# Kernel optimization log

Hardware: AMD Instinct MI355X
Metric: run time of the kernel (lower is better)

## Reference

```python
import jax, jax.numpy as jnp
import numpy as np

B, N, E = 128, 196, 2048   # batch, num_features (14x14), encoder_dim
D, A = 512, 512            # decoder_dim, attention_dim


def setup_inputs() -> dict:
    key = jax.random.key(0)
    ks = jax.random.split(key, 8)
    s_e = 1.0 / np.sqrt(E)
    s_d = 1.0 / np.sqrt(D)
    s_a = 1.0 / np.sqrt(A)
    return {
        "encoder_out": jax.random.normal(ks[0], (B, N, E), dtype=jnp.float32),
        "decoder_hidden": jax.random.normal(ks[1], (B, D), dtype=jnp.float32),
        "We": jax.random.uniform(ks[2], (E, A), jnp.float32, -s_e, s_e),
        "be": jax.random.uniform(ks[3], (A,), jnp.float32, -s_e, s_e),
        "Wd": jax.random.uniform(ks[4], (D, A), jnp.float32, -s_d, s_d),
        "bd": jax.random.uniform(ks[5], (A,), jnp.float32, -s_d, s_d),
        "Wf": jax.random.uniform(ks[6], (A, 1), jnp.float32, -s_a, s_a),
        "bf": jax.random.uniform(ks[7], (1,), jnp.float32, -s_a, s_a),
    }


def reference(encoder_out, decoder_hidden, We, be, Wd, bd, Wf, bf):
    # att1: [B,N,A] projection of encoder features
    att1 = jnp.einsum('bne,ea->bna', encoder_out, We) + be
    # att2: [B,A] projection of decoder state, broadcast over N
    att2 = decoder_hidden @ Wd + bd
    att = jnp.tanh(att1 + att2[:, None, :])          # [B,N,A]
    scores = jnp.einsum('bna,ao->bno', att, Wf) + bf  # [B,N,1]
    alpha = jax.nn.softmax(scores, axis=1)            # softmax over num_features
    context = jnp.sum(encoder_out * alpha, axis=1)    # [B,E]
    return (context, alpha)
```

## Files before the change

### kernel.cpp

```cpp
#include <hip/hip_runtime.h>
#include <hip/hip_bf16.h>
#include <stdint.h>

#define B_   128
#define N_   196
#define E_   2048
#define D_   512
#define A_   512
#define MTOT (B_ * N_)

typedef short  short8  __attribute__((ext_vector_type(8)));
typedef float  floatx4 __attribute__((ext_vector_type(4)));

__device__ __forceinline__ unsigned short f2bf(float f) {
    union { float f; uint32_t u; } v; v.f = f;
    uint32_t r = v.u + 0x7FFFu + ((v.u >> 16) & 1u);
    return (unsigned short)(r >> 16);
}

__device__ __forceinline__ uint32_t pkbf(float a, float b) {
    uint32_t ua = __float_as_uint(a) + 0x8000u;
    uint32_t ub = __float_as_uint(b) + 0x8000u;
    return __builtin_amdgcn_perm(ub, ua, 0x07060302u);
}

__global__ void transcvt_k(const float* __restrict__ We, unsigned short* __restrict__ WeT) {
    __shared__ float tile[32][33];
    const int e0 = blockIdx.x * 32, a0 = blockIdx.y * 32;
    const int t = threadIdx.x, tc = t & 31, tr = t >> 5;
#pragma unroll
    for (int i = 0; i < 4; ++i) {
        int r = tr + i * 8;
        tile[r][tc] = We[(size_t)(e0 + r) * A_ + a0 + tc];
    }
    __syncthreads();
#pragma unroll
    for (int i = 0; i < 4; ++i) {
        int r = tr + i * 8;
        WeT[(size_t)(a0 + r) * E_ + e0 + tc] = f2bf(tile[tc][r]);
    }
}

__launch_bounds__(512)
__global__ void att2_k(const float* __restrict__ dh, const float* __restrict__ Wd,
                       const float* __restrict__ bd, const float* __restrict__ be,
                       float* __restrict__ att2p) {
    const int b = blockIdx.x, t = threadIdx.x;
    __shared__ float sdh[D_];
    sdh[t] = dh[b * D_ + t];
    __syncthreads();
    float acc = 0.f;
#pragma unroll 8
    for (int d = 0; d < D_; ++d) acc += sdh[d] * Wd[(size_t)d * A_ + t];
    att2p[(size_t)b * A_ + t] = acc + bd[t] + be[t];
}

__launch_bounds__(512, 4)
__global__ void score_gemm(const float* __restrict__ enc,
                           const unsigned short* __restrict__ WeT,
                           const float* __restrict__ att2p,
                           const float* __restrict__ Wf,
                           float* __restrict__ scoresP) {
    __shared__ __align__(16) char sMem[8192 + 32768];
    __shared__ float sPart[8][64];

    const int t   = threadIdx.x;
    const int w   = t >> 6;
    const int l   = t & 63;
    const int l15 = l & 15;
    const int q4  = l >> 4;
    const int row0 = blockIdx.x * 64;

    floatx4 acc[4][4] = {};

    const float* aSrc;
    int aDst;
    {
        int s = w * 64 + l;
        int r = s >> 3, p = s & 7;
        aSrc = enc + (size_t)(row0 + r) * E_ + ((p ^ (r & 7)) * 4);
        aDst = w * 1024;
    }
    const unsigned short* bSrc[4];
    int bDst[4];
#pragma unroll
    for (int j = 0; j < 4; ++j) {
        int s = (w * 4 + j) * 64 + l;
        int n = s >> 2, p = s & 3;
        int q = p ^ ((n >> 1) & 3);
        bSrc[j] = WeT + (size_t)n * E_ + q * 8;
        bDst[j] = 8192 + (w * 4 + j) * 1024;
    }

    const int pLo   = (2 * q4) ^ (l15 & 7);
    const int offAlo = l15 * 128 + pLo * 16;
    const int offAhi = l15 * 128 + (pLo ^ 1) * 16;
    const int offB   = 8192 + (w * 64 + l15) * 64 + (q4 ^ ((l15 >> 1) & 3)) * 16;

    for (int kk = 0; kk < 64; ++kk) {
        __builtin_amdgcn_global_load_lds(
            (const __attribute__((address_space(1))) uint32_t*)(aSrc + kk * 32),
            (__attribute__((address_space(3))) uint32_t*)(sMem + aDst), 16, 0, 0);
#pragma unroll
        for (int j = 0; j < 4; ++j)
            __builtin_amdgcn_global_load_lds(
                (const __attribute__((address_space(1))) uint32_t*)(bSrc[j] + kk * 32),
                (__attribute__((address_space(3))) uint32_t*)(sMem + bDst[j]), 16, 0, 0);
        __syncthreads();

        short8 bfr[4];
        union { uint32_t u[4]; short8 s; } af[4];
#pragma unroll
        for (int ni = 0; ni < 4; ++ni)
            bfr[ni] = *(const short8*)(sMem + offB + ni * 1024);
#pragma unroll
        for (int mi = 0; mi < 4; ++mi) {
            float4 lo = *(const float4*)(sMem + offAlo + mi * 2048);
            float4 hi = *(const float4*)(sMem + offAhi + mi * 2048);
            af[mi].u[0] = pkbf(lo.x, lo.y);
            af[mi].u[1] = pkbf(lo.z, lo.w);
            af[mi].u[2] = pkbf(hi.x, hi.y);
            af[mi].u[3] = pkbf(hi.z, hi.w);
        }
#pragma unroll
        for (int mi = 0; mi < 4; ++mi) {
            acc[mi][0] = __builtin_amdgcn_mfma_f32_16x16x32_bf16(af[mi].s, bfr[0], acc[mi][0], 0, 0, 0);
            acc[mi][1] = __builtin_amdgcn_mfma_f32_16x16x32_bf16(af[mi].s, bfr[1], acc[mi][1], 0, 0, 0);
            acc[mi][2] = __builtin_amdgcn_mfma_f32_16x16x32_bf16(af[mi].s, bfr[2], acc[mi][2], 0, 0, 0);
            acc[mi][3] = __builtin_amdgcn_mfma_f32_16x16x32_bf16(af[mi].s, bfr[3], acc[mi][3], 0, 0, 0);
        }
        __syncthreads();
    }

    const int cbase = w * 64;
    float wfv[4];
#pragma unroll
    for (int ni = 0; ni < 4; ++ni) wfv[ni] = Wf[cbase + ni * 16 + l15];

#pragma unroll
    for (int mi = 0; mi < 4; ++mi) {
#pragma unroll
        for (int r = 0; r < 4; ++r) {
            const int m    = mi * 16 + q4 * 4 + r;
            const int grow = row0 + m;
            const int bb   = grow / N_;
            const float* a2 = att2p + (size_t)bb * A_ + cbase;
            float s = 0.f;
#pragma unroll
            for (int ni = 0; ni < 4; ++ni) {
                float v  = acc[mi][ni][r] + a2[ni * 16 + l15];
                float e  = __expf(2.f * v);
                float th = 1.f - 2.f / (e + 1.f);
                s += th * wfv[ni];
            }
            s += __shfl_xor(s, 1);
            s += __shfl_xor(s, 2);
            s += __shfl_xor(s, 4);
            s += __shfl_xor(s, 8);
            if (l15 == 0) sPart[w][m] = s;
        }
    }
    __syncthreads();
    if (t < 64) {
        float v = 0.f;
#pragma unroll
        for (int ww = 0; ww < 8; ++ww) v += sPart[ww][t];
        scoresP[row0 + t] = v;
    }
}

__global__ void softmax_k(const float* __restrict__ sp, float* __restrict__ alpha) {
    const int b = blockIdx.x, t = threadIdx.x;
    const int w = t >> 6, l = t & 63;
    __shared__ float red[8];
    float v = -3.0e38f;
    if (t < N_) v = sp[b * N_ + t];
    float m = v;
#pragma unroll
    for (int off = 32; off >= 1; off >>= 1) m = fmaxf(m, __shfl_xor(m, off));
    if (l == 0) red[w] = m;
    __syncthreads();
    m = fmaxf(fmaxf(red[0], red[1]), fmaxf(red[2], red[3]));
    float e = 0.f;
    if (t < N_) e = __expf(v - m);
    float s = e;
#pragma unroll
    for (int off = 32; off >= 1; off >>= 1) s += __shfl_xor(s, off);
    if (l == 0) red[4 + w] = s;
    __syncthreads();
    s = red[4] + red[5] + red[6] + red[7];
    if (t < N_) alpha[b * N_ + t] = e / s;
}

__launch_bounds__(256)
__global__ void context_k(const float* __restrict__ enc, const float* __restrict__ alpha,
                          float* __restrict__ ctx) {
    const int chunk = blockIdx.x, b = blockIdx.y;
    const int t = threadIdx.x, tn = t >> 6, tc = t & 63;
    __shared__ float  sAl[N_];
    __shared__ float4 sRed[256];
    if (t < N_) sAl[t] = alpha[b * N_ + t];
    __syncthreads();
    const float* base = enc + (size_t)b * N_ * E_ + chunk * 256 + tc * 4;
    float4 a = make_float4(0.f, 0.f, 0.f, 0.f);
#pragma unroll 7
    for (int n = tn; n < N_; n += 4) {
        float  al = sAl[n];
        float4 v  = *(const float4*)(base + (size_t)n * E_);
        a.x += al * v.x; a.y += al * v.y; a.z += al * v.z; a.w += al * v.w;
    }
    sRed[t] = a;
    __syncthreads();
    if (t < 64) {
        float4 r0 = sRed[t], r1 = sRed[t + 64], r2 = sRed[t + 128], r3 = sRed[t + 192];
        float4 o = make_float4(r0.x + r1.x + r2.x + r3.x, r0.y + r1.y + r2.y + r3.y,
                               r0.z + r1.z + r2.z + r3.z, r0.w + r1.w + r2.w + r3.w);
        *(float4*)(ctx + (size_t)b * E_ + chunk * 256 + t * 4) = o;
    }
}

extern "C" void kernel_launch(void* const* d_in, const int* in_sizes, int n_in,
                              void* d_out, int out_size, void* d_ws, size_t ws_size,
                              hipStream_t stream) {
    const float* enc = (const float*)d_in[0];
    const float* dh  = (const float*)d_in[1];
    const float* We  = (const float*)d_in[2];
    const float* be  = (const float*)d_in[3];
    const float* Wd  = (const float*)d_in[4];
    const float* bd  = (const float*)d_in[5];
    const float* Wf  = (const float*)d_in[6];

    float* out   = (float*)d_out;
    float* ctx   = out;
    float* alpha = out + B_ * E_;

    char* ws = (char*)d_ws;
    unsigned short* WeT  = (unsigned short*)ws;
    float* att2p         = (float*)(ws + (2u << 20));
    float* scoresP       = (float*)(ws + (2u << 20) + (256u << 10));

    transcvt_k <<<dim3(E_ / 32, A_ / 32), 256, 0, stream>>>(We, WeT);
    att2_k     <<<dim3(B_),              512, 0, stream>>>(dh, Wd, bd, be, att2p);
    score_gemm <<<dim3(MTOT / 64),       512, 0, stream>>>(enc, WeT, att2p, Wf, scoresP);
    softmax_k  <<<dim3(B_),              256, 0, stream>>>(scoresP, alpha);
    context_k  <<<dim3(E_ / 256, B_),    256, 0, stream>>>(enc, alpha, ctx);
}
```

Before: 441.9 us.

## Double-buffer score GEMM LDS and pre-convert encoder tile to bf16 once

The score GEMM now keeps two LDS buffers and prefetches the next k-slice of both operands while MFMAs run on the current one, which removes one barrier per iteration and hides global latency. The fp32 encoder tile is loaded through registers, packed to bf16 once by the loading thread and stored into a swizzled bf16 LDS layout. Each wave therefore no longer converts shared fp32 data redundantly, and the A tile in LDS shrinks. In exchange, LDS use per block grows to about 72KB, which may lower occupancy relative to the launch bounds of 4 blocks, and the register-routed A loads add VGPR pressure.

```diff
diff --git a/kernel.cpp b/kernel.cpp
--- a/kernel.cpp
+++ b/kernel.cpp
@@ -61,7 +61,7 @@
                            const float* __restrict__ att2p,
                            const float* __restrict__ Wf,
                            float* __restrict__ scoresP) {
-    __shared__ __align__(16) char sMem[8192 + 32768];
+    __shared__ __align__(16) char sMem[2 * 36864];
     __shared__ float sPart[8][64];
 
     const int t   = threadIdx.x;
@@ -73,14 +73,10 @@
 
     floatx4 acc[4][4] = {};
 
-    const float* aSrc;
-    int aDst;
-    {
-        int s = w * 64 + l;
-        int r = s >> 3, p = s & 7;
-        aSrc = enc + (size_t)(row0 + r) * E_ + ((p ^ (r & 7)) * 4);
-        aDst = w * 1024;
-    }
+    const int ar = t >> 3, ap = t & 7;
+    const float* aSrcT = enc + (size_t)(row0 + ar) * E_ + ap * 4;
+    const int aWr = ar * 64 + (((ap >> 1) ^ ((ar >> 1) & 3)) * 16) + (ap & 1) * 8;
+
     const unsigned short* bSrc[4];
     int bDst[4];
 #pragma unroll
@@ -89,47 +85,59 @@
         int n = s >> 2, p = s & 3;
         int q = p ^ ((n >> 1) & 3);
         bSrc[j] = WeT + (size_t)n * E_ + q * 8;
-        bDst[j] = 8192 + (w * 4 + j) * 1024;
-    }
-
-    const int pLo   = (2 * q4) ^ (l15 & 7);
-    const int offAlo = l15 * 128 + pLo * 16;
-    const int offAhi = l15 * 128 + (pLo ^ 1) * 16;
-    const int offB   = 8192 + (w * 64 + l15) * 64 + (q4 ^ ((l15 >> 1) & 3)) * 16;
-
-    for (int kk = 0; kk < 64; ++kk) {
-        __builtin_amdgcn_global_load_lds(
-            (const __attribute__((address_space(1))) uint32_t*)(aSrc + kk * 32),
-            (__attribute__((address_space(3))) uint32_t*)(sMem + aDst), 16, 0, 0);
+        bDst[j] = 4096 + (w * 4 + j) * 1024;
+    }
+
+    const int chA  = q4 ^ ((l15 >> 1) & 3);
+    const int offA = l15 * 64 + chA * 16;
+    const int offB = 4096 + (w * 64 + l15) * 64 + chA * 16;
+
+    {
+        float4 a0 = *(const float4*)(aSrcT);
 #pragma unroll
         for (int j = 0; j < 4; ++j)
             __builtin_amdgcn_global_load_lds(
-                (const __attribute__((address_space(1))) uint32_t*)(bSrc[j] + kk * 32),
+                (const __attribute__((address_space(1))) uint32_t*)(bSrc[j]),
                 (__attribute__((address_space(3))) uint32_t*)(sMem + bDst[j]), 16, 0, 0);
+        uint2 aw;
+        aw.x = pkbf(a0.x, a0.y);
+        aw.y = pkbf(a0.z, a0.w);
+        *(uint2*)(sMem + aWr) = aw;
         __syncthreads();
+    }
+
+    int cur = 0;
+#pragma unroll 2
+    for (int kk = 0; kk < 64; ++kk) {
+        const int nxt = cur ^ 36864;
+        const int kn  = (kk + 1) & 63;
+
+        float4 aNext = *(const float4*)(aSrcT + kn * 32);
+#pragma unroll
+        for (int j = 0; j < 4; ++j)
+            __builtin_amdgcn_global_load_lds(
+                (const __attribute__((address_space(1))) uint32_t*)(bSrc[j] + kn * 32),
+                (__attribute__((address_space(3))) uint32_t*)(sMem + nxt + bDst[j]), 16, 0, 0);
 
         short8 bfr[4];
-        union { uint32_t u[4]; short8 s; } af[4];
 #pragma unroll
         for (int ni = 0; ni < 4; ++ni)
-            bfr[ni] = *(const short8*)(sMem + offB + ni * 1024);
+            bfr[ni] = *(const short8*)(sMem + cur + offB + ni * 1024);
 #pragma unroll
         for (int mi = 0; mi < 4; ++mi) {
-            float4 lo = *(const float4*)(sMem + offAlo + mi * 2048);
-            float4 hi = *(const float4*)(sMem + offAhi + mi * 2048);
-            af[mi].u[0] = pkbf(lo.x, lo.y);
-            af[mi].u[1] = pkbf(lo.z, lo.w);
-            af[mi].u[2] = pkbf(hi.x, hi.y);
-            af[mi].u[3] = pkbf(hi.z, hi.w);
+            short8 a = *(const short8*)(sMem + cur + offA + mi * 1024);
+            acc[mi][0] = __builtin_amdgcn_mfma_f32_16x16x32_bf16(a, bfr[0], acc[mi][0], 0, 0, 0);
+            acc[mi][1] = __builtin_amdgcn_mfma_f32_16x16x32_bf16(a, bfr[1], acc[mi][1], 0, 0, 0);
+            acc[mi][2] = __builtin_amdgcn_mfma_f32_16x16x32_bf16(a, bfr[2], acc[mi][2], 0, 0, 0);
+            acc[mi][3] = __builtin_amdgcn_mfma_f32_16x16x32_bf16(a, bfr[3], acc[mi][3], 0, 0, 0);
         }
-#pragma unroll
-        for (int mi = 0; mi < 4; ++mi) {
-            acc[mi][0] = __builtin_amdgcn_mfma_f32_16x16x32_bf16(af[mi].s, bfr[0], acc[mi][0], 0, 0, 0);
-            acc[mi][1] = __builtin_amdgcn_mfma_f32_16x16x32_bf16(af[mi].s, bfr[1], acc[mi][1], 0, 0, 0);
-            acc[mi][2] = __builtin_amdgcn_mfma_f32_16x16x32_bf16(af[mi].s, bfr[2], acc[mi][2], 0, 0, 0);
-            acc[mi][3] = __builtin_amdgcn_mfma_f32_16x16x32_bf16(af[mi].s, bfr[3], acc[mi][3], 0, 0, 0);
-        }
+
+        uint2 aw;
+        aw.x = pkbf(aNext.x, aNext.y);
+        aw.y = pkbf(aNext.z, aNext.w);
+        *(uint2*)(sMem + nxt + aWr) = aw;
         __syncthreads();
+        cur = nxt;
     }
 
     const int cbase = w * 64;
```

Measured after the change: 420.1 us. -4.9%, faster.
